# Kernel optimization log

Measured on AMD Instinct MI355X. Metric: run time of the kernel, lower is better.

Reference implementation:

```python
import math
import jax, jax.numpy as jnp
import numpy as np

NUM_HEADS = 32
NUM_KV_HEADS = 8
HEAD_DIM = 128
HIDDEN = 4096
ROPE_THETA = 500000.0
ROPE_FACTOR = 8.0
HIGH_FF = 4.0
LOW_FF = 1.0
ORIG_MAX_POS = 8192


def _llama3_inv_freq():
    # Llama-3 rope frequency scaling
    inv = 1.0 / (ROPE_THETA ** (np.arange(0, HEAD_DIM, 2, dtype=np.float32) / HEAD_DIM))
    wavelen = 2.0 * np.pi / inv
    low_wl = ORIG_MAX_POS / LOW_FF
    high_wl = ORIG_MAX_POS / HIGH_FF
    inv_scaled = np.where(wavelen > low_wl, inv / ROPE_FACTOR, inv)
    smooth = (ORIG_MAX_POS / wavelen - LOW_FF) / (HIGH_FF - LOW_FF)
    smoothed = (1.0 - smooth) / ROPE_FACTOR * inv + smooth * inv
    is_medium = (wavelen <= low_wl) & (wavelen >= high_wl)
    return jnp.asarray(np.where(is_medium, smoothed, inv_scaled), dtype=jnp.float32)


def _rotate_half(x):
    h = x.shape[-1] // 2
    return jnp.concatenate([-x[..., h:], x[..., :h]], axis=-1)


def setup_inputs() -> dict:
    key = jax.random.key(0)
    ks = jax.random.split(key, 5)
    s = 0.02
    return {
        "x": jax.random.normal(ks[0], (1, 2048, HIDDEN), dtype=jnp.float32),
        "Wq": jax.random.normal(ks[1], (NUM_HEADS * HEAD_DIM, HIDDEN), dtype=jnp.float32) * s,
        "Wk": jax.random.normal(ks[2], (NUM_KV_HEADS * HEAD_DIM, HIDDEN), dtype=jnp.float32) * s,
        "Wv": jax.random.normal(ks[3], (NUM_KV_HEADS * HEAD_DIM, HIDDEN), dtype=jnp.float32) * s,
        "Wo": jax.random.normal(ks[4], (HIDDEN, NUM_HEADS * HEAD_DIM), dtype=jnp.float32) * s,
    }


def reference(x, Wq, Wk, Wv, Wo):
    B, T, _ = x.shape
    G = NUM_HEADS // NUM_KV_HEADS  # query heads per kv head

    q = jnp.einsum("bth,oh->bto", x, Wq).reshape(B, T, NUM_HEADS, HEAD_DIM).transpose(0, 2, 1, 3)
    k = jnp.einsum("bth,oh->bto", x, Wk).reshape(B, T, NUM_KV_HEADS, HEAD_DIM).transpose(0, 2, 1, 3)
    v = jnp.einsum("bth,oh->bto", x, Wv).reshape(B, T, NUM_KV_HEADS, HEAD_DIM).transpose(0, 2, 1, 3)

    # RoPE (past_len = 0, prefill)
    inv_freq = _llama3_inv_freq()
    pos = jnp.arange(T, dtype=jnp.float32)
    freqs = pos[:, None] * inv_freq[None, :]             # [T, D/2]
    emb = jnp.concatenate([freqs, freqs], axis=-1)       # [T, D]
    cos, sin = jnp.cos(emb), jnp.sin(emb)
    q = q * cos + _rotate_half(q) * sin
    k = k * cos + _rotate_half(k) * sin

    # GQA attention: group query heads over kv heads instead of repeat_interleave
    qg = q.reshape(B, NUM_KV_HEADS, G, T, HEAD_DIM)
    scale = 1.0 / math.sqrt(HEAD_DIM)
    scores = jnp.einsum("bkgtd,bksd->bkgts", qg, k) * scale  # [B,Hkv,G,T,T]
    causal = jnp.tril(jnp.ones((T, T), dtype=bool))
    scores = jnp.where(causal, scores, -jnp.inf)
    attn = jax.nn.softmax(scores, axis=-1)
    out = jnp.einsum("bkgts,bksd->bkgtd", attn, v)           # [B,Hkv,G,T,D]
    out = out.reshape(B, NUM_HEADS, T, HEAD_DIM).transpose(0, 2, 1, 3).reshape(B, T, NUM_HEADS * HEAD_DIM)
    return jnp.einsum("bto,ho->bth", out, Wo)
```

## Files before the change

### kernel.cpp

```cpp
#include <hip/hip_runtime.h>
#include <math.h>

#define T 2048
#define HID 4096
#define NH 32
#define NKV 8
#define HD 128
#define QSCALE 0.08838834764831845f

typedef __attribute__((ext_vector_type(8))) short short8;
typedef __attribute__((ext_vector_type(4))) float f32x4;
typedef __attribute__((ext_vector_type(16))) float f32x16;

static __device__ __forceinline__ unsigned short f2bf(float f) {
  union { float f; unsigned u; } v; v.f = f;
  unsigned r = v.u;
  r += 0x7fffu + ((r >> 16) & 1u);
  return (unsigned short)(r >> 16);
}

static __device__ __forceinline__ void async_cp16(const unsigned short* g, unsigned short* l) {
  __builtin_amdgcn_global_load_lds(
      (const __attribute__((address_space(1))) void*)g,
      (__attribute__((address_space(3))) void*)l,
      16, 0, 0);
}

__global__ __launch_bounds__(256) void cast4_kernel(const float* __restrict__ s0, const float* __restrict__ s1,
                                                    const float* __restrict__ s2, const float* __restrict__ s3,
                                                    unsigned short* __restrict__ d0, unsigned short* __restrict__ d1,
                                                    unsigned short* __restrict__ d2, unsigned short* __restrict__ d3,
                                                    int n0, int n1, int n2, int n3) {
  int i = blockIdx.x * 256 + threadIdx.x;
  const float* s; unsigned short* d; int j = i;
  if (j < n0) { s = s0; d = d0; }
  else { j -= n0;
    if (j < n1) { s = s1; d = d1; }
    else { j -= n1;
      if (j < n2) { s = s2; d = d2; }
      else { j -= n2;
        if (j >= n3) return;
        s = s3; d = d3; } } }
  float4 f = ((const float4*)s)[j];
  ushort4 o;
  o.x = f2bf(f.x); o.y = f2bf(f.y); o.z = f2bf(f.z); o.w = f2bf(f.w);
  ((ushort4*)d)[j] = o;
}

__global__ __launch_bounds__(256) void cast_bf16_kernel(const float* __restrict__ src,
                                                        unsigned short* __restrict__ dst,
                                                        int n4) {
  int i = blockIdx.x * 256 + threadIdx.x;
  if (i >= n4) return;
  float4 f = ((const float4*)src)[i];
  ushort4 o;
  o.x = f2bf(f.x); o.y = f2bf(f.y); o.z = f2bf(f.z); o.w = f2bf(f.w);
  ((ushort4*)dst)[i] = o;
}


static __device__ __forceinline__ short8 ldfrag(const unsigned short* tile, int row0, int ks, int lane) {
  int row = row0 + (lane & 15);
  int slot = (ks * 4 + (lane >> 4)) ^ (lane & 7);
  return *(const short8*)&tile[row * 64 + slot * 8];
}

static __device__ __forceinline__ void ldb2(short8 (&b)[2][2], const unsigned short* bs, int br0, int lane) {
#pragma unroll
  for (int j = 0; j < 2; j++)
#pragma unroll
    for (int ks = 0; ks < 2; ks++)
      b[j][ks] = ldfrag(bs, br0 + j * 16, ks, lane);
}

template <int H>
static __device__ __forceinline__ void preA(short8 (&a)[4][2], const unsigned short* as, int ar, int lane) {
#pragma unroll
  for (int m = 2 * H; m < 2 * H + 2; m++)
#pragma unroll
    for (int ks = 0; ks < 2; ks++)
      a[m][ks] = ldfrag(as, ar + m * 16, ks, lane);
}

template <int P, int NF>
static __device__ __forceinline__ void mfma16(const short8 (&a)[4][2], const short8 (&b)[2][2],
                                              f32x4 (&acc)[4][2 * NF]) {
  __builtin_amdgcn_s_setprio(1);
#pragma unroll
  for (int ks = 0; ks < 2; ks++)
#pragma unroll
    for (int m = 0; m < 4; m++)
#pragma unroll
      for (int j = 0; j < 2; j++)
        acc[m][P * 2 + j] = __builtin_amdgcn_mfma_f32_16x16x32_bf16(
            a[m][ks], b[j][ks], acc[m][P * 2 + j], 0, 0, 0);
  __builtin_amdgcn_s_setprio(0);
}

#define SCHED0 __builtin_amdgcn_sched_barrier(0)
#define BAR_PRE  do { SCHED0; __builtin_amdgcn_s_barrier(); \
                      asm volatile("s_waitcnt lgkmcnt(0)" ::: "memory"); SCHED0; } while (0)
#define BAR_POST do { SCHED0; __builtin_amdgcn_s_barrier(); SCHED0; } while (0)
#define VMCNT(n) asm volatile("s_waitcnt vmcnt(" #n ")" ::: "memory")

template <int NF>
static __device__ __forceinline__ void tile_body(
    short8 (&aC)[4][2], short8 (&aN)[4][2],
    const unsigned short* bsRd, unsigned short* bsSt,
    const unsigned short* asN, unsigned short* asS,
    const unsigned short* const (&baseA)[4], const unsigned short* const (&baseB)[NF],
    int kA, int kB, int ar, int br, int wave, int lane,
    f32x4 (&acc)[4][2 * NF]) {
  short8 b[2][2];
  if constexpr (NF == 3) {
    ldb2(b, bsRd, br + 0, lane);
    async_cp16(baseB[0] + kB, bsSt + 0 * 4096 + wave * 512);
    async_cp16(baseB[1] + kB, bsSt + 1 * 4096 + wave * 512);
    async_cp16(baseB[2] + kB, bsSt + 2 * 4096 + wave * 512);
    BAR_PRE; mfma16<0, NF>(aC, b, acc); BAR_POST;
    ldb2(b, bsRd, br + 32, lane);
    preA<0>(aN, asN, ar, lane);
    async_cp16(baseA[0] + kA, asS + 0 * 4096 + wave * 512);
    async_cp16(baseA[1] + kA, asS + 1 * 4096 + wave * 512);
    BAR_PRE; mfma16<1, NF>(aC, b, acc); BAR_POST;
    ldb2(b, bsRd, br + 64, lane);
    preA<1>(aN, asN, ar, lane);
    async_cp16(baseA[2] + kA, asS + 2 * 4096 + wave * 512);
    async_cp16(baseA[3] + kA, asS + 3 * 4096 + wave * 512);
    VMCNT(4);
    BAR_PRE; mfma16<2, NF>(aC, b, acc); BAR_POST;
  } else {
    ldb2(b, bsRd, br + 0, lane);
    preA<0>(aN, asN, ar, lane);
    async_cp16(baseB[0] + kB, bsSt + 0 * 4096 + wave * 512);
    async_cp16(baseB[1] + kB, bsSt + 1 * 4096 + wave * 512);
    BAR_PRE; mfma16<0, NF>(aC, b, acc); BAR_POST;
    ldb2(b, bsRd, br + 32, lane);
    preA<1>(aN, asN, ar, lane);
    async_cp16(baseA[0] + kA, asS + 0 * 4096 + wave * 512);
    async_cp16(baseA[1] + kA, asS + 1 * 4096 + wave * 512);
    async_cp16(baseA[2] + kA, asS + 2 * 4096 + wave * 512);
    async_cp16(baseA[3] + kA, asS + 3 * 4096 + wave * 512);
    VMCNT(6);
    BAR_PRE; mfma16<1, NF>(aC, b, acc); BAR_POST;
  }
}

template <int NF>
__global__ __launch_bounds__(512, 2) void gemm9(const unsigned short* __restrict__ A,
                                                const unsigned short* __restrict__ Bt,
                                                float* __restrict__ C,
                                                int M, int N, int K) {
  __shared__ __align__(16) unsigned short AsBuf[3][16384];
  __shared__ __align__(16) unsigned short BsBuf[NF == 3 ? 2 : 3][NF * 4096];
  int tid = threadIdx.x, wave = tid >> 6, lane = tid & 63;
  int wm = wave >> 1, wn = wave & 1;
  long bm0 = (long)blockIdx.y * 256, bn0 = (long)blockIdx.x * (NF * 64);
  int ar = wm * 64, br = wn * (NF * 32);

  long stRow = wave * 8 + (lane >> 3);
  int slot = ((lane & 7) ^ (lane >> 3)) * 8;
  const unsigned short* baseA[4];
#pragma unroll
  for (int c = 0; c < 4; c++) baseA[c] = A + (bm0 + c * 64 + stRow) * (long)K + slot;
  const unsigned short* baseB[NF];
#pragma unroll
  for (int c = 0; c < NF; c++) baseB[c] = Bt + (bn0 + c * 64 + stRow) * (long)K + slot;

  int nkt = K >> 6;
  f32x4 acc[4][2 * NF] = {};
  short8 aX[4][2], aY[4][2];
  unsigned short *as0 = AsBuf[0], *as1 = AsBuf[1], *as2 = AsBuf[2];

  if constexpr (NF == 3) {
#pragma unroll
    for (int c = 0; c < 3; c++) async_cp16(baseB[c], &BsBuf[0][c * 4096 + wave * 512]);
#pragma unroll
    for (int c = 0; c < 4; c++) async_cp16(baseA[c], as0 + c * 4096 + wave * 512);
#pragma unroll
    for (int c = 0; c < 4; c++) async_cp16(baseA[c] + 64, as1 + c * 4096 + wave * 512);
#pragma unroll
    for (int c = 0; c < 4; c++) async_cp16(baseA[c] + 128, as2 + c * 4096 + wave * 512);
    VMCNT(4);
    SCHED0; __builtin_amdgcn_s_barrier(); SCHED0;
    preA<0>(aX, as0, ar, lane); preA<1>(aX, as0, ar, lane);
#pragma unroll 1
    for (int it = 0; it < (nkt >> 1); ++it) {
      int t = 2 * it;
      int kA0 = ((t + 3) < nkt ? (t + 3) : (nkt - 1)) << 6;
      int kB0 = ((t + 1) < nkt ? (t + 1) : (nkt - 1)) << 6;
      tile_body<3>(aX, aY, BsBuf[0], BsBuf[1], as1, as0, baseA, baseB, kA0, kB0, ar, br, wave, lane, acc);
      int kA1 = ((t + 4) < nkt ? (t + 4) : (nkt - 1)) << 6;
      int kB1 = ((t + 2) < nkt ? (t + 2) : (nkt - 1)) << 6;
      tile_body<3>(aY, aX, BsBuf[1], BsBuf[0], as2, as1, baseA, baseB, kA1, kB1, ar, br, wave, lane, acc);
      unsigned short* tA = as0; as0 = as2; as2 = as1; as1 = tA;
    }
  } else {
    unsigned short *bs0 = BsBuf[0], *bs1 = BsBuf[1], *bs2 = BsBuf[2];
#pragma unroll
    for (int c = 0; c < 2; c++) async_cp16(baseB[c], bs0 + c * 4096 + wave * 512);
#pragma unroll
    for (int c = 0; c < 4; c++) async_cp16(baseA[c], as0 + c * 4096 + wave * 512);
#pragma unroll
    for (int c = 0; c < 2; c++) async_cp16(baseB[c] + 64, bs1 + c * 4096 + wave * 512);
#pragma unroll
    for (int c = 0; c < 4; c++) async_cp16(baseA[c] + 64, as1 + c * 4096 + wave * 512);
#pragma unroll
    for (int c = 0; c < 4; c++) async_cp16(baseA[c] + 128, as2 + c * 4096 + wave * 512);
    VMCNT(4);
    SCHED0; __builtin_amdgcn_s_barrier(); SCHED0;
    preA<0>(aX, as0, ar, lane); preA<1>(aX, as0, ar, lane);
#pragma unroll 1
    for (int it = 0; it < (nkt >> 1); ++it) {
      int t = 2 * it;
      int kA0 = ((t + 3) < nkt ? (t + 3) : (nkt - 1)) << 6;
      int kB0 = ((t + 2) < nkt ? (t + 2) : (nkt - 1)) << 6;
      tile_body<2>(aX, aY, bs0, bs2, as1, as0, baseA, baseB, kA0, kB0, ar, br, wave, lane, acc);
      int kA1 = ((t + 4) < nkt ? (t + 4) : (nkt - 1)) << 6;
      int kB1 = ((t + 3) < nkt ? (t + 3) : (nkt - 1)) << 6;
      tile_body<2>(aY, aX, bs1, bs0, as2, as1, baseA, baseB, kA1, kB1, ar, br, wave, lane, acc);
      unsigned short* tA = as0; as0 = as2; as2 = as1; as1 = tA;
      unsigned short* tB = bs0; bs0 = bs2; bs2 = bs1; bs1 = tB;
    }
  }
  VMCNT(0);

#pragma unroll
  for (int m = 0; m < 4; m++)
#pragma unroll
    for (int n = 0; n < 2 * NF; n++) {
      long row = bm0 + ar + m * 16 + ((lane >> 4) << 2);
      long col = bn0 + br + n * 16 + (lane & 15);
#pragma unroll
      for (int j = 0; j < 4; j++)
        C[(row + j) * (long)N + col] = acc[m][n][j];
    }
}

__global__ __launch_bounds__(64) void rope_qk(const float* __restrict__ qkvf,
                                              unsigned short* __restrict__ qb,
                                              unsigned short* __restrict__ kb) {
  int t = blockIdx.x, hh = blockIdx.y, d = threadIdx.x;
  float ex = (float)d * (1.0f / 64.0f);
  float inv = expf(-ex * 13.122363377404328f);
  float wl = 6.283185307179586f / inv;
  float inv_s;
  if (wl > 8192.0f)       inv_s = inv * 0.125f;
  else if (wl < 2048.0f)  inv_s = inv;
  else {
    float smooth = (8192.0f / wl - 1.0f) * (1.0f / 3.0f);
    inv_s = (1.0f - smooth) * 0.125f * inv + smooth * inv;
  }
  float ang = (float)t * inv_s;
  float s, c;
  sincosf(ang, &s, &c);
  if (hh < NH) {
    const float* base = qkvf + (long)t * 6144 + hh * HD;
    float lo = base[d], hi = base[d + 64];
    long o = ((long)hh * T + t) * HD;
    qb[o + d]      = f2bf((lo * c - hi * s) * QSCALE);
    qb[o + d + 64] = f2bf((hi * c + lo * s) * QSCALE);
  } else {
    int h = hh - NH;
    const float* base = qkvf + (long)t * 6144 + 4096 + h * HD;
    float lo = base[d], hi = base[d + 64];
    long o = ((long)h * T + t) * HD;
    kb[o + d]      = f2bf(lo * c - hi * s);
    kb[o + d + 64] = f2bf(hi * c + lo * s);
  }
}

__global__ __launch_bounds__(256) void transpose_v(const float* __restrict__ qkvf,
                                                   unsigned short* __restrict__ vtb) {
  __shared__ float tile[64][33];
  int t0 = blockIdx.x * 64, d0 = blockIdx.y * 32, h = blockIdx.z;
  int tid = threadIdx.x;
  int dd = tid & 31, tt = tid >> 5;
#pragma unroll
  for (int i = 0; i < 8; i++) {
    int t = tt + i * 8;
    tile[t][dd] = qkvf[(long)(t0 + t) * 6144 + 5120 + h * HD + d0 + dd];
  }
  __syncthreads();
  int t2 = tid & 63, d2 = tid >> 6;
#pragma unroll
  for (int i = 0; i < 8; i++) {
    int d = d2 + i * 4;
    vtb[((long)(h * HD + d0 + d)) * T + t0 + t2] = f2bf(tile[t2][d]);
  }
}

__global__ __launch_bounds__(256, 2) void attn_kernel(const unsigned short* __restrict__ qb,
                                                      const unsigned short* __restrict__ kbuf,
                                                      const unsigned short* __restrict__ vtb,
                                                      unsigned short* __restrict__ ob) {
  __shared__ __align__(16) unsigned short Ks[64 * 128];
  __shared__ __align__(16) unsigned short Vs[128 * 64];
  __shared__ __align__(16) unsigned short Ps[4][32 * 76];
  int h = blockIdx.y;
  int kvh = h >> 2;
  int qt = (blockIdx.y >= 16) ? (int)(gridDim.x - 1 - blockIdx.x) : (int)blockIdx.x;
  int q0 = qt * 128;
  int tid = threadIdx.x, wave = tid >> 6, lane = tid & 63;
  int l31 = lane & 31, half = lane >> 5;
  const unsigned short* Kb = kbuf + (long)kvh * T * HD;
  const unsigned short* Vb = vtb + (long)kvh * HD * T;

  int qrow = q0 + wave * 32 + l31;
  short8 aq[8];
#pragma unroll
  for (int ks = 0; ks < 8; ks++)
    aq[ks] = *(const short8*)&qb[((long)h * T + qrow) * HD + ks * 16 + half * 8];

  f32x16 oacc[4] = {};
  float psum[16];
#pragma unroll
  for (int r = 0; r < 16; r++) psum[r] = 0.0f;

  int ntiles = 2 * qt + 2;
  for (int tile = 0; tile < ntiles; tile++) {
    int kb0 = tile * 64;
#pragma unroll
    for (int i = 0; i < 4; i++) {
      int c = wave * 4 + i;
      { int row = c * 4 + (lane >> 4);
        int g = (lane & 15) ^ (row & 15);
        async_cp16(&Kb[(long)(kb0 + row) * HD + g * 8], &Ks[c * 512]); }
      { int row = c * 8 + (lane >> 3);
        int g = (lane & 7) ^ (row & 7);
        async_cp16(&Vb[(long)row * T + kb0 + g * 8], &Vs[c * 512]); }
    }
    __syncthreads();

    f32x16 sacc[2] = {};
#pragma unroll
    for (int ks = 0; ks < 8; ks++)
#pragma unroll
      for (int nt = 0; nt < 2; nt++) {
        int row = nt * 32 + l31;
        short8 bk = *(const short8*)&Ks[row * 128 + (((2 * ks + half) ^ (row & 15)) * 8)];
        sacc[nt] = __builtin_amdgcn_mfma_f32_32x32x16_bf16(aq[ks], bk, sacc[nt], 0, 0, 0);
      }

    if (kb0 + 63 > q0 + wave * 32) {
#pragma unroll
      for (int nt = 0; nt < 2; nt++) {
        int key = kb0 + nt * 32 + l31;
#pragma unroll
        for (int r = 0; r < 16; r++) {
          int qr = q0 + wave * 32 + (r & 3) + 8 * (r >> 2) + 4 * half;
          if (key > qr) sacc[nt][r] = -3.0e38f;
        }
      }
    }

#pragma unroll
    for (int nt = 0; nt < 2; nt++)
#pragma unroll
      for (int r = 0; r < 16; r++) {
        float p = __expf(sacc[nt][r]);
        psum[r] += p;
        int prow = (r & 3) + 8 * (r >> 2) + 4 * half;
        Ps[wave][prow * 76 + nt * 32 + l31] = f2bf(p);
      }

#pragma unroll
    for (int ks = 0; ks < 4; ks++) {
      short8 ap = *(const short8*)&Ps[wave][l31 * 76 + ks * 16 + half * 8];
#pragma unroll
      for (int nt = 0; nt < 4; nt++) {
        int row = nt * 32 + l31;
        short8 bv = *(const short8*)&Vs[row * 64 + (((2 * ks + half) ^ (row & 7)) * 8)];
        oacc[nt] = __builtin_amdgcn_mfma_f32_32x32x16_bf16(ap, bv, oacc[nt], 0, 0, 0);
      }
    }
    __syncthreads();
  }

#pragma unroll
  for (int off = 1; off <= 16; off <<= 1)
#pragma unroll
    for (int r = 0; r < 16; r++)
      psum[r] += __shfl_xor(psum[r], off, 64);

#pragma unroll
  for (int nt = 0; nt < 4; nt++)
#pragma unroll
    for (int r = 0; r < 16; r++) {
      int row = q0 + wave * 32 + (r & 3) + 8 * (r >> 2) + 4 * half;
      ob[(long)row * HID + h * HD + nt * 32 + l31] = f2bf(oacc[nt][r] / psum[r]);
    }
}

extern "C" void kernel_launch(void* const* d_in, const int* in_sizes, int n_in,
                              void* d_out, int out_size, void* d_ws, size_t ws_size,
                              hipStream_t stream) {
  const float* x  = (const float*)d_in[0];
  const float* Wq = (const float*)d_in[1];
  const float* Wk = (const float*)d_in[2];
  const float* Wv = (const float*)d_in[3];
  const float* Wo = (const float*)d_in[4];
  float* out = (float*)d_out;

  char* ws = (char*)d_ws;
  size_t off = 0;
  auto alloc = [&](size_t bytes) {
    char* p = ws + off;
    off += (bytes + 255) & ~(size_t)255;
    return p;
  };
  unsigned short* x_bf    = (unsigned short*)alloc((size_t)T * HID * 2);
  unsigned short* wqkv_bf = (unsigned short*)alloc((size_t)6144 * HID * 2);
  float* qkvf = (float*)alloc((size_t)T * 6144 * 4);
  unsigned short* qb  = (unsigned short*)alloc((size_t)NH * T * HD * 2);
  unsigned short* kbb = (unsigned short*)alloc((size_t)NKV * T * HD * 2);
  unsigned short* vtb = (unsigned short*)alloc((size_t)NKV * HD * T * 2);
  unsigned short* obb = (unsigned short*)alloc((size_t)T * HID * 2);

  int n0 = T * HID / 4, n1 = HID * HID / 4, n2 = 1024 * HID / 4, n3 = 1024 * HID / 4;
  int ntot = n0 + n1 + n2 + n3;
  cast4_kernel<<<dim3((ntot + 255) / 256), dim3(256), 0, stream>>>(
      x, Wq, Wk, Wv,
      x_bf, wqkv_bf, wqkv_bf + (size_t)HID * HID, wqkv_bf + (size_t)5120 * HID,
      n0, n1, n2, n3);

  gemm9<3><<<dim3(6144 / 192, T / 256), dim3(512), 0, stream>>>(x_bf, wqkv_bf, qkvf, T, 6144, HID);

  rope_qk<<<dim3(T, NH + NKV), dim3(64), 0, stream>>>(qkvf, qb, kbb);
  transpose_v<<<dim3(T / 64, HD / 32, NKV), dim3(256), 0, stream>>>(qkvf, vtb);

  cast_bf16_kernel<<<dim3((HID * HID / 4 + 255) / 256), dim3(256), 0, stream>>>(Wo, wqkv_bf, HID * HID / 4);
  attn_kernel<<<dim3(T / 128, NH), dim3(256), 0, stream>>>(qb, kbb, vtb, obb);
  gemm9<2><<<dim3(HID / 128, T / 256), dim3(512), 0, stream>>>(obb, wqkv_bf, out, T, HID, HID);
}
```

Measured before the change: 461.5 us.

## Double-buffer K/V tiles in attention kernel and XOR-swizzle P staging buffer

Splits K and V shared-memory tiles into two buffers so the next tile's async global-to-LDS copy is issued before computing on the current one. Waits use explicit vmcnt counts with raw barriers instead of a full syncthreads. Also replaces the padded P buffer (stride 76) with a stride-64 layout using an XOR swizzle to avoid bank conflicts. Doubling K/V LDS raises shared memory use per block to about 80KB, which may limit occupancy with launch_bounds(256,2). The vmcnt(8) count depends on the exact number of outstanding loads, including the Q loads.

```diff
diff --git a/kernel.cpp b/kernel.cpp
--- a/kernel.cpp
+++ b/kernel.cpp
@@ -294,9 +294,9 @@
                                                       const unsigned short* __restrict__ kbuf,
                                                       const unsigned short* __restrict__ vtb,
                                                       unsigned short* __restrict__ ob) {
-  __shared__ __align__(16) unsigned short Ks[64 * 128];
-  __shared__ __align__(16) unsigned short Vs[128 * 64];
-  __shared__ __align__(16) unsigned short Ps[4][32 * 76];
+  __shared__ __align__(16) unsigned short Ks[2][64 * 128];
+  __shared__ __align__(16) unsigned short Vs[2][128 * 64];
+  __shared__ __align__(16) unsigned short Ps[4][32 * 64];
   int h = blockIdx.y;
   int kvh = h >> 2;
   int qt = (blockIdx.y >= 16) ? (int)(gridDim.x - 1 - blockIdx.x) : (int)blockIdx.x;
@@ -306,31 +306,43 @@
   const unsigned short* Kb = kbuf + (long)kvh * T * HD;
   const unsigned short* Vb = vtb + (long)kvh * HD * T;
 
-  int qrow = q0 + wave * 32 + l31;
-  short8 aq[8];
-#pragma unroll
-  for (int ks = 0; ks < 8; ks++)
-    aq[ks] = *(const short8*)&qb[((long)h * T + qrow) * HD + ks * 16 + half * 8];
-
-  f32x16 oacc[4] = {};
-  float psum[16];
-#pragma unroll
-  for (int r = 0; r < 16; r++) psum[r] = 0.0f;
-
-  int ntiles = 2 * qt + 2;
-  for (int tile = 0; tile < ntiles; tile++) {
+  auto STAGE = [&](int tile, int bf) {
     int kb0 = tile * 64;
 #pragma unroll
     for (int i = 0; i < 4; i++) {
       int c = wave * 4 + i;
       { int row = c * 4 + (lane >> 4);
         int g = (lane & 15) ^ (row & 15);
-        async_cp16(&Kb[(long)(kb0 + row) * HD + g * 8], &Ks[c * 512]); }
+        async_cp16(&Kb[(long)(kb0 + row) * HD + g * 8], &Ks[bf][c * 512]); }
       { int row = c * 8 + (lane >> 3);
         int g = (lane & 7) ^ (row & 7);
-        async_cp16(&Vb[(long)row * T + kb0 + g * 8], &Vs[c * 512]); }
-    }
-    __syncthreads();
+        async_cp16(&Vb[(long)row * T + kb0 + g * 8], &Vs[bf][c * 512]); }
+    }
+  };
+
+  STAGE(0, 0);
+
+  int qrow = q0 + wave * 32 + l31;
+  short8 aq[8];
+#pragma unroll
+  for (int ks = 0; ks < 8; ks++)
+    aq[ks] = *(const short8*)&qb[((long)h * T + qrow) * HD + ks * 16 + half * 8];
+
+  f32x16 oacc[4] = {};
+  float psum[16];
+#pragma unroll
+  for (int r = 0; r < 16; r++) psum[r] = 0.0f;
+
+  int ntiles = 2 * qt + 2;
+  for (int tile = 0; tile < ntiles; tile++) {
+    int cur = tile & 1;
+    if (tile + 1 < ntiles) {
+      STAGE(tile + 1, cur ^ 1);
+      asm volatile("s_waitcnt vmcnt(8)" ::: "memory");
+    } else {
+      asm volatile("s_waitcnt vmcnt(0)" ::: "memory");
+    }
+    SCHED0; __builtin_amdgcn_s_barrier(); SCHED0;
 
     f32x16 sacc[2] = {};
 #pragma unroll
@@ -338,10 +350,11 @@
 #pragma unroll
       for (int nt = 0; nt < 2; nt++) {
         int row = nt * 32 + l31;
-        short8 bk = *(const short8*)&Ks[row * 128 + (((2 * ks + half) ^ (row & 15)) * 8)];
+        short8 bk = *(const short8*)&Ks[cur][row * 128 + (((2 * ks + half) ^ (row & 15)) * 8)];
         sacc[nt] = __builtin_amdgcn_mfma_f32_32x32x16_bf16(aq[ks], bk, sacc[nt], 0, 0, 0);
       }
 
+    int kb0 = tile * 64;
     if (kb0 + 63 > q0 + wave * 32) {
 #pragma unroll
       for (int nt = 0; nt < 2; nt++) {
@@ -361,20 +374,20 @@
         float p = __expf(sacc[nt][r]);
         psum[r] += p;
         int prow = (r & 3) + 8 * (r >> 2) + 4 * half;
-        Ps[wave][prow * 76 + nt * 32 + l31] = f2bf(p);
+        Ps[wave][prow * 64 + ((nt * 32 + l31) ^ ((prow & 7) << 3))] = f2bf(p);
       }
 
 #pragma unroll
     for (int ks = 0; ks < 4; ks++) {
-      short8 ap = *(const short8*)&Ps[wave][l31 * 76 + ks * 16 + half * 8];
+      short8 ap = *(const short8*)&Ps[wave][l31 * 64 + (((ks * 2 + half) ^ (l31 & 7)) * 8)];
 #pragma unroll
       for (int nt = 0; nt < 4; nt++) {
         int row = nt * 32 + l31;
-        short8 bv = *(const short8*)&Vs[row * 64 + (((2 * ks + half) ^ (row & 7)) * 8)];
+        short8 bv = *(const short8*)&Vs[cur][row * 64 + (((2 * ks + half) ^ (row & 7)) * 8)];
         oacc[nt] = __builtin_amdgcn_mfma_f32_32x32x16_bf16(ap, bv, oacc[nt], 0, 0, 0);
       }
     }
-    __syncthreads();
+    SCHED0; __builtin_amdgcn_s_barrier(); SCHED0;
   }
 
 #pragma unroll
```

After: 452.5 us. No clear change (-1.9%).
